# Performance work log

Hardware: AMD Instinct MI355X
Metric: run time of the kernel (lower is better)

## Reference

```python
import jax, jax.numpy as jnp
import numpy as np

N = 500_000
B = 10_000
L = N // B  # 50 tokens per session
H = 128


def setup_inputs() -> dict:
    key = jax.random.key(0)
    ks = jax.random.split(key, 7)
    x = jax.random.normal(ks[0], (N, H), dtype=jnp.float32)
    # sorted segment ids: B sessions of length L (every segment non-empty)
    batch = jnp.repeat(jnp.arange(B, dtype=jnp.int32), L)
    # index of the last element of each session
    last_ixs = jnp.arange(B, dtype=jnp.int32) * L + (L - 1)
    s = 1.0 / np.sqrt(H)
    W1_w = jax.random.uniform(ks[1], (H, H), jnp.float32, -s, s)
    W1_b = jax.random.uniform(ks[2], (H,), jnp.float32, -s, s)
    W2_w = jax.random.uniform(ks[3], (H, H), jnp.float32, -s, s)
    W2_b = jax.random.uniform(ks[4], (H,), jnp.float32, -s, s)
    q_w = jax.random.uniform(ks[5], (1, H), jnp.float32, -s, s)
    q_b = jax.random.uniform(ks[6], (1,), jnp.float32, -s, s)
    return {"x": x, "W1_w": W1_w, "W1_b": W1_b, "W2_w": W2_w, "W2_b": W2_b,
            "q_w": q_w, "q_b": q_b, "batch": batch, "last_ixs": last_ixs,
            "num_segments": B}


def reference(x, W1_w, W1_b, W2_w, W2_b, q_w, q_b, batch, last_ixs, num_segments):
    # v_i = x[last_ixs]; repeat_interleave(v_i, bincount(batch)) == v_i[batch] (batch sorted)
    v_n_repeat = x[last_ixs][batch]                                   # [N, H]
    h = jax.nn.sigmoid(v_n_repeat @ W1_w.T + W1_b + x @ W2_w.T + W2_b)  # [N, H]
    e = (h @ q_w.T + q_b)[:, 0]                                       # [N]
    # segment-wise (per-session) numerically-stable softmax
    m = jax.ops.segment_max(e, batch, num_segments=num_segments)      # [B]
    z = jnp.exp(e - m[batch])                                         # [N]
    denom = jax.ops.segment_sum(z, batch, num_segments=num_segments)  # [B]
    alpha = (z / denom[batch])[:, None]                               # [N, 1]
    # scatter_add pooling of alpha * x over sessions
    s_g = jax.ops.segment_sum(alpha * x, batch, num_segments=num_segments)  # [B, H]
    return s_g
```

## Files before the change

### kernel.cpp

```cpp
#include <hip/hip_runtime.h>

#define H_DIM 128
#define L_SESS 50
#define B_SESS 10000
#define M_PAD 64
#define LDSTR 136
#define PSTR 68

typedef __bf16 bf16x8 __attribute__((ext_vector_type(8)));
typedef float f32x4 __attribute__((ext_vector_type(4)));

static __device__ __forceinline__ unsigned short f2bf(float f) {
  unsigned int u = __float_as_uint(f);
  u += 0x7FFFu + ((u >> 16) & 1u);
  return (unsigned short)(u >> 16);
}
static __device__ __forceinline__ float bf2f(unsigned short h) {
  return __uint_as_float(((unsigned int)h) << 16);
}

__global__ __launch_bounds__(256) void cvt_w2_kernel(
    const float* __restrict__ w2, unsigned short* __restrict__ w2b) {
  int i = blockIdx.x * 256 + threadIdx.x;
  float4 v = ((const float4*)w2)[i];
  ushort4 o;
  o.x = f2bf(v.x); o.y = f2bf(v.y); o.z = f2bf(v.z); o.w = f2bf(v.w);
  *(ushort4*)(w2b + (size_t)i * 4) = o;
}

__global__ __launch_bounds__(256) void sess_u_kernel(
    const float* __restrict__ x, const float* __restrict__ w1,
    const float* __restrict__ w1b, const float* __restrict__ w2bias,
    float* __restrict__ U) {
  __shared__ __attribute__((aligned(16))) unsigned short W1s[H_DIM * LDSTR];
  __shared__ __attribute__((aligned(16))) unsigned short Vs[16 * LDSTR];
  const int t = threadIdx.x;
  const int s0 = blockIdx.x * 16;

  for (int i = t; i < 4096; i += 256) {
    float4 v = ((const float4*)w1)[i];
    int row = i >> 5;
    int col = (i & 31) * 4;
    ushort4 o;
    o.x = f2bf(v.x); o.y = f2bf(v.y); o.z = f2bf(v.z); o.w = f2bf(v.w);
    *(ushort4*)&W1s[row * LDSTR + col] = o;
  }
  for (int i = t; i < 512; i += 256) {
    int j = i >> 5;
    int col = (i & 31) * 4;
    float4 v = ((const float4*)(x + ((size_t)(s0 + j) * L_SESS + (L_SESS - 1)) * H_DIM))[i & 31];
    ushort4 o;
    o.x = f2bf(v.x); o.y = f2bf(v.y); o.z = f2bf(v.z); o.w = f2bf(v.w);
    *(ushort4*)&Vs[j * LDSTR + col] = o;
  }
  __syncthreads();

  const int lane = t & 63, w = t >> 6, q = lane >> 4, c = lane & 15;
  const int n0 = (w * 2) * 16 + c;
  const int n1 = (w * 2 + 1) * 16 + c;
  f32x4 acc0 = {0.f, 0.f, 0.f, 0.f};
  f32x4 acc1 = {0.f, 0.f, 0.f, 0.f};
#pragma unroll
  for (int kt = 0; kt < 4; ++kt) {
    bf16x8 a  = *(const bf16x8*)&Vs[c * LDSTR + kt * 32 + q * 8];
    bf16x8 b0 = *(const bf16x8*)&W1s[n0 * LDSTR + kt * 32 + q * 8];
    bf16x8 b1 = *(const bf16x8*)&W1s[n1 * LDSTR + kt * 32 + q * 8];
    acc0 = __builtin_amdgcn_mfma_f32_16x16x32_bf16(a, b0, acc0, 0, 0, 0);
    acc1 = __builtin_amdgcn_mfma_f32_16x16x32_bf16(a, b1, acc1, 0, 0, 0);
  }
  float bias0 = w1b[n0] + w2bias[n0];
  float bias1 = w1b[n1] + w2bias[n1];
#pragma unroll
  for (int r = 0; r < 4; ++r) {
    int m = q * 4 + r;
    U[(size_t)(s0 + m) * H_DIM + n0] = acc0[r] + bias0;
    U[(size_t)(s0 + m) * H_DIM + n1] = acc1[r] + bias1;
  }
}

__global__ __launch_bounds__(256) void sess_attn_kernel(
    const float* __restrict__ x, const unsigned short* __restrict__ W2b,
    const float* __restrict__ U, const float* __restrict__ qw,
    const float* __restrict__ qb, float* __restrict__ out) {
  __shared__ __attribute__((aligned(16))) unsigned short Wb[H_DIM * LDSTR];
  __shared__ __attribute__((aligned(16))) unsigned short Xb[M_PAD * LDSTR];
  __shared__ float alpha_s[M_PAD];
  float* psc = (float*)Wb;

  const int t = threadIdx.x;
  const int b = blockIdx.x;
  const int lane = t & 63, w = t >> 6, q = lane >> 4, c = lane & 15;
  const int n0 = (w * 2) * 16 + c;
  const int n1 = (w * 2 + 1) * 16 + c;

  const float un0 = U[(size_t)b * H_DIM + n0];
  const float un1 = U[(size_t)b * H_DIM + n1];
  const float qn0 = qw[n0];
  const float qn1 = qw[n1];
  const float qbv = qb[0];

  for (int i = t; i < 2048; i += 256) {
    uint4 v = ((const uint4*)W2b)[i];
    int row = i >> 4;
    int col = (i & 15) * 8;
    *(uint4*)&Wb[row * LDSTR + col] = v;
  }
  const float* xs = x + (size_t)b * (L_SESS * H_DIM);
  for (int i = t; i < 1600; i += 256) {
    float4 v = ((const float4*)xs)[i];
    int row = i >> 5;
    int col = (i & 31) * 4;
    ushort4 o;
    o.x = f2bf(v.x); o.y = f2bf(v.y); o.z = f2bf(v.z); o.w = f2bf(v.w);
    *(ushort4*)&Xb[row * LDSTR + col] = o;
  }
  __syncthreads();

  f32x4 acc[4][2];
  const f32x4 zero4 = {0.f, 0.f, 0.f, 0.f};
#pragma unroll
  for (int mt = 0; mt < 4; ++mt) { acc[mt][0] = zero4; acc[mt][1] = zero4; }
#pragma unroll
  for (int kt = 0; kt < 4; ++kt) {
    bf16x8 a[4];
#pragma unroll
    for (int mt = 0; mt < 4; ++mt)
      a[mt] = *(const bf16x8*)&Xb[(mt * 16 + c) * LDSTR + kt * 32 + q * 8];
    bf16x8 b0 = *(const bf16x8*)&Wb[n0 * LDSTR + kt * 32 + q * 8];
    bf16x8 b1 = *(const bf16x8*)&Wb[n1 * LDSTR + kt * 32 + q * 8];
#pragma unroll
    for (int mt = 0; mt < 4; ++mt) {
      acc[mt][0] = __builtin_amdgcn_mfma_f32_16x16x32_bf16(a[mt], b0, acc[mt][0], 0, 0, 0);
      acc[mt][1] = __builtin_amdgcn_mfma_f32_16x16x32_bf16(a[mt], b1, acc[mt][1], 0, 0, 0);
    }
  }
  __syncthreads();

#pragma unroll
  for (int mt = 0; mt < 4; ++mt) {
#pragma unroll
    for (int r = 0; r < 4; ++r) {
      float t0 = acc[mt][0][r] + un0;
      float t1 = acc[mt][1][r] + un1;
      float h0 = 1.0f / (1.0f + __expf(-t0));
      float h1 = 1.0f / (1.0f + __expf(-t1));
      int row = mt * 16 + q * 4 + r;
      psc[row * PSTR + w * 16 + c] = h0 * qn0 + h1 * qn1;
    }
  }
  __syncthreads();

  if (t < 64) {
    const float4* prow = (const float4*)(psc + t * PSTR);
    float s = 0.f;
#pragma unroll
    for (int j = 0; j < 16; ++j) {
      float4 v4 = prow[j];
      s += (v4.x + v4.y) + (v4.z + v4.w);
    }
    float e = s + qbv;
    float val = (t < L_SESS) ? e : -1.0e30f;
    float mx = val;
#pragma unroll
    for (int off = 32; off > 0; off >>= 1) mx = fmaxf(mx, __shfl_xor(mx, off));
    float z = (t < L_SESS) ? __expf(e - mx) : 0.f;
    float d = z;
#pragma unroll
    for (int off = 32; off > 0; off >>= 1) d += __shfl_xor(d, off);
    alpha_s[t] = z / d;
  }
  __syncthreads();

  if (t < 64) {
    float s0 = 0.f, s1 = 0.f;
    for (int m = 0; m < L_SESS; ++m) {
      unsigned int pv = *(const unsigned int*)&Xb[m * LDSTR + 2 * t];
      float a = alpha_s[m];
      s0 += a * bf2f((unsigned short)(pv & 0xFFFFu));
      s1 += a * bf2f((unsigned short)(pv >> 16));
    }
    float2 o2;
    o2.x = s0;
    o2.y = s1;
    *(float2*)(out + (size_t)b * H_DIM + 2 * t) = o2;
  }
}

extern "C" void kernel_launch(void* const* d_in, const int* in_sizes, int n_in,
                              void* d_out, int out_size, void* d_ws, size_t ws_size,
                              hipStream_t stream) {
  const float* x    = (const float*)d_in[0];
  const float* w1   = (const float*)d_in[1];
  const float* w1b  = (const float*)d_in[2];
  const float* w2   = (const float*)d_in[3];
  const float* w2bi = (const float*)d_in[4];
  const float* qw   = (const float*)d_in[5];
  const float* qb   = (const float*)d_in[6];
  float* out = (float*)d_out;

  unsigned short* W2bf = (unsigned short*)d_ws;
  float* U = out;

  cvt_w2_kernel<<<16, 256, 0, stream>>>(w2, W2bf);
  sess_u_kernel<<<B_SESS / 16, 256, 0, stream>>>(x, w1, w1b, w2bi, U);
  sess_attn_kernel<<<B_SESS, 256, 0, stream>>>(x, W2bf, U, qw, qb, out);
}
```

Before: 423.3 us.

## Fuse session-vector GEMM into attention kernel and keep W2 in registers

Removes the separate sess_u kernel by computing the last-token W1 projection inside each attention block with a small MFMA on the already-staged row 49. W2 fragments now load straight from global memory into registers rather than being staged through a 34KB LDS tile, which cuts LDS use and allows a higher occupancy hint. The partial score reduction moves to warp shuffles, and the final pooling re-reads fp32 x from global memory with all 256 threads. The trade-off is redundant W1 work per session, since only row 0 of each 16-row MFMA tile is used, plus extra global and L2 traffic for the pooling pass and for W1/W2 fragment loads in every block.

```diff
diff --git a/kernel.cpp b/kernel.cpp
--- a/kernel.cpp
+++ b/kernel.cpp
@@ -3,162 +3,111 @@
 #define H_DIM 128
 #define L_SESS 50
 #define B_SESS 10000
-#define M_PAD 64
 #define LDSTR 136
-#define PSTR 68
+#define ESTR 5
 
+typedef __bf16 bf16_t;
 typedef __bf16 bf16x8 __attribute__((ext_vector_type(8)));
 typedef float f32x4 __attribute__((ext_vector_type(4)));
 
-static __device__ __forceinline__ unsigned short f2bf(float f) {
-  unsigned int u = __float_as_uint(f);
-  u += 0x7FFFu + ((u >> 16) & 1u);
-  return (unsigned short)(u >> 16);
-}
-static __device__ __forceinline__ float bf2f(unsigned short h) {
-  return __uint_as_float(((unsigned int)h) << 16);
+__global__ __launch_bounds__(256) void cvt_kernel(
+    const float* __restrict__ w1, const float* __restrict__ w2,
+    const float* __restrict__ w1b, const float* __restrict__ w2bi,
+    unsigned short* __restrict__ wout, float* __restrict__ bias12) {
+  int i = blockIdx.x * 256 + threadIdx.x;
+  float4 v = (i < 4096) ? ((const float4*)w1)[i] : ((const float4*)w2)[i - 4096];
+  union { bf16_t h[4]; ushort4 u4; } tmp;
+  tmp.h[0] = (bf16_t)v.x; tmp.h[1] = (bf16_t)v.y;
+  tmp.h[2] = (bf16_t)v.z; tmp.h[3] = (bf16_t)v.w;
+  *(ushort4*)(wout + (size_t)4 * i) = tmp.u4;
+  if (i < H_DIM) bias12[i] = w1b[i] + w2bi[i];
 }
 
-__global__ __launch_bounds__(256) void cvt_w2_kernel(
-    const float* __restrict__ w2, unsigned short* __restrict__ w2b) {
-  int i = blockIdx.x * 256 + threadIdx.x;
-  float4 v = ((const float4*)w2)[i];
-  ushort4 o;
-  o.x = f2bf(v.x); o.y = f2bf(v.y); o.z = f2bf(v.z); o.w = f2bf(v.w);
-  *(ushort4*)(w2b + (size_t)i * 4) = o;
-}
-
-__global__ __launch_bounds__(256) void sess_u_kernel(
-    const float* __restrict__ x, const float* __restrict__ w1,
-    const float* __restrict__ w1b, const float* __restrict__ w2bias,
-    float* __restrict__ U) {
-  __shared__ __attribute__((aligned(16))) unsigned short W1s[H_DIM * LDSTR];
-  __shared__ __attribute__((aligned(16))) unsigned short Vs[16 * LDSTR];
-  const int t = threadIdx.x;
-  const int s0 = blockIdx.x * 16;
-
-  for (int i = t; i < 4096; i += 256) {
-    float4 v = ((const float4*)w1)[i];
-    int row = i >> 5;
-    int col = (i & 31) * 4;
-    ushort4 o;
-    o.x = f2bf(v.x); o.y = f2bf(v.y); o.z = f2bf(v.z); o.w = f2bf(v.w);
-    *(ushort4*)&W1s[row * LDSTR + col] = o;
-  }
-  for (int i = t; i < 512; i += 256) {
-    int j = i >> 5;
-    int col = (i & 31) * 4;
-    float4 v = ((const float4*)(x + ((size_t)(s0 + j) * L_SESS + (L_SESS - 1)) * H_DIM))[i & 31];
-    ushort4 o;
-    o.x = f2bf(v.x); o.y = f2bf(v.y); o.z = f2bf(v.z); o.w = f2bf(v.w);
-    *(ushort4*)&Vs[j * LDSTR + col] = o;
-  }
-  __syncthreads();
-
-  const int lane = t & 63, w = t >> 6, q = lane >> 4, c = lane & 15;
-  const int n0 = (w * 2) * 16 + c;
-  const int n1 = (w * 2 + 1) * 16 + c;
-  f32x4 acc0 = {0.f, 0.f, 0.f, 0.f};
-  f32x4 acc1 = {0.f, 0.f, 0.f, 0.f};
-#pragma unroll
-  for (int kt = 0; kt < 4; ++kt) {
-    bf16x8 a  = *(const bf16x8*)&Vs[c * LDSTR + kt * 32 + q * 8];
-    bf16x8 b0 = *(const bf16x8*)&W1s[n0 * LDSTR + kt * 32 + q * 8];
-    bf16x8 b1 = *(const bf16x8*)&W1s[n1 * LDSTR + kt * 32 + q * 8];
-    acc0 = __builtin_amdgcn_mfma_f32_16x16x32_bf16(a, b0, acc0, 0, 0, 0);
-    acc1 = __builtin_amdgcn_mfma_f32_16x16x32_bf16(a, b1, acc1, 0, 0, 0);
-  }
-  float bias0 = w1b[n0] + w2bias[n0];
-  float bias1 = w1b[n1] + w2bias[n1];
-#pragma unroll
-  for (int r = 0; r < 4; ++r) {
-    int m = q * 4 + r;
-    U[(size_t)(s0 + m) * H_DIM + n0] = acc0[r] + bias0;
-    U[(size_t)(s0 + m) * H_DIM + n1] = acc1[r] + bias1;
-  }
-}
-
-__global__ __launch_bounds__(256) void sess_attn_kernel(
-    const float* __restrict__ x, const unsigned short* __restrict__ W2b,
-    const float* __restrict__ U, const float* __restrict__ qw,
+__global__ __launch_bounds__(256, 4) void sess_attn_kernel(
+    const float* __restrict__ x, const unsigned short* __restrict__ Wb,
+    const float* __restrict__ bias12, const float* __restrict__ qw,
     const float* __restrict__ qb, float* __restrict__ out) {
-  __shared__ __attribute__((aligned(16))) unsigned short Wb[H_DIM * LDSTR];
-  __shared__ __attribute__((aligned(16))) unsigned short Xb[M_PAD * LDSTR];
-  __shared__ float alpha_s[M_PAD];
-  float* psc = (float*)Wb;
+  __shared__ __attribute__((aligned(16))) unsigned short Xb[64 * LDSTR];
+  __shared__ float epart[64 * ESTR];
+  __shared__ float alpha_s[64];
+  __shared__ float pool_s[H_DIM];
 
   const int t = threadIdx.x;
   const int b = blockIdx.x;
   const int lane = t & 63, w = t >> 6, q = lane >> 4, c = lane & 15;
-  const int n0 = (w * 2) * 16 + c;
-  const int n1 = (w * 2 + 1) * 16 + c;
+  const int n0 = w * 32 + c;
+  const int n1 = w * 32 + 16 + c;
 
-  const float un0 = U[(size_t)b * H_DIM + n0];
-  const float un1 = U[(size_t)b * H_DIM + n1];
-  const float qn0 = qw[n0];
-  const float qn1 = qw[n1];
-  const float qbv = qb[0];
+  const float* xs = x + (size_t)b * (L_SESS * H_DIM);
+  const bf16x8* W1v = (const bf16x8*)(Wb);
+  const bf16x8* W2v = (const bf16x8*)(Wb + 16384);
 
-  for (int i = t; i < 2048; i += 256) {
-    uint4 v = ((const uint4*)W2b)[i];
-    int row = i >> 4;
-    int col = (i & 15) * 8;
-    *(uint4*)&Wb[row * LDSTR + col] = v;
+  bf16x8 bw2[4][2];
+#pragma unroll
+  for (int kt = 0; kt < 4; ++kt) {
+    bw2[kt][0] = W2v[(n0 * H_DIM + kt * 32 + q * 8) >> 3];
+    bw2[kt][1] = W2v[(n1 * H_DIM + kt * 32 + q * 8) >> 3];
   }
-  const float* xs = x + (size_t)b * (L_SESS * H_DIM);
+  const float bias0 = bias12[n0], bias1 = bias12[n1];
+  const float qn0 = qw[n0], qn1 = qw[n1], qbv = qb[0];
+
   for (int i = t; i < 1600; i += 256) {
     float4 v = ((const float4*)xs)[i];
-    int row = i >> 5;
-    int col = (i & 31) * 4;
-    ushort4 o;
-    o.x = f2bf(v.x); o.y = f2bf(v.y); o.z = f2bf(v.z); o.w = f2bf(v.w);
-    *(ushort4*)&Xb[row * LDSTR + col] = o;
+    int row = i >> 5, col = (i & 31) * 4;
+    union { bf16_t h[4]; ushort4 u4; } tmp;
+    tmp.h[0] = (bf16_t)v.x; tmp.h[1] = (bf16_t)v.y;
+    tmp.h[2] = (bf16_t)v.z; tmp.h[3] = (bf16_t)v.w;
+    *(ushort4*)&Xb[row * LDSTR + col] = tmp.u4;
   }
   __syncthreads();
 
+  const f32x4 zero4 = {0.f, 0.f, 0.f, 0.f};
+
+  f32x4 accu[2] = {zero4, zero4};
+#pragma unroll
+  for (int kt = 0; kt < 4; ++kt) {
+    bf16x8 av = *(const bf16x8*)&Xb[49 * LDSTR + kt * 32 + q * 8];
+    accu[0] = __builtin_amdgcn_mfma_f32_16x16x32_bf16(
+        av, W1v[(n0 * H_DIM + kt * 32 + q * 8) >> 3], accu[0], 0, 0, 0);
+    accu[1] = __builtin_amdgcn_mfma_f32_16x16x32_bf16(
+        av, W1v[(n1 * H_DIM + kt * 32 + q * 8) >> 3], accu[1], 0, 0, 0);
+  }
+  const float u0 = accu[0][0] + bias0;
+  const float u1 = accu[1][0] + bias1;
+
   f32x4 acc[4][2];
-  const f32x4 zero4 = {0.f, 0.f, 0.f, 0.f};
 #pragma unroll
   for (int mt = 0; mt < 4; ++mt) { acc[mt][0] = zero4; acc[mt][1] = zero4; }
 #pragma unroll
   for (int kt = 0; kt < 4; ++kt) {
-    bf16x8 a[4];
-#pragma unroll
-    for (int mt = 0; mt < 4; ++mt)
-      a[mt] = *(const bf16x8*)&Xb[(mt * 16 + c) * LDSTR + kt * 32 + q * 8];
-    bf16x8 b0 = *(const bf16x8*)&Wb[n0 * LDSTR + kt * 32 + q * 8];
-    bf16x8 b1 = *(const bf16x8*)&Wb[n1 * LDSTR + kt * 32 + q * 8];
 #pragma unroll
     for (int mt = 0; mt < 4; ++mt) {
-      acc[mt][0] = __builtin_amdgcn_mfma_f32_16x16x32_bf16(a[mt], b0, acc[mt][0], 0, 0, 0);
-      acc[mt][1] = __builtin_amdgcn_mfma_f32_16x16x32_bf16(a[mt], b1, acc[mt][1], 0, 0, 0);
+      bf16x8 a = *(const bf16x8*)&Xb[(mt * 16 + c) * LDSTR + kt * 32 + q * 8];
+      acc[mt][0] = __builtin_amdgcn_mfma_f32_16x16x32_bf16(a, bw2[kt][0], acc[mt][0], 0, 0, 0);
+      acc[mt][1] = __builtin_amdgcn_mfma_f32_16x16x32_bf16(a, bw2[kt][1], acc[mt][1], 0, 0, 0);
     }
   }
-  __syncthreads();
 
 #pragma unroll
   for (int mt = 0; mt < 4; ++mt) {
 #pragma unroll
     for (int r = 0; r < 4; ++r) {
-      float t0 = acc[mt][0][r] + un0;
-      float t1 = acc[mt][1][r] + un1;
+      float t0 = acc[mt][0][r] + u0;
+      float t1 = acc[mt][1][r] + u1;
       float h0 = 1.0f / (1.0f + __expf(-t0));
       float h1 = 1.0f / (1.0f + __expf(-t1));
-      int row = mt * 16 + q * 4 + r;
-      psc[row * PSTR + w * 16 + c] = h0 * qn0 + h1 * qn1;
+      float p = h0 * qn0 + h1 * qn1;
+#pragma unroll
+      for (int off = 1; off <= 8; off <<= 1) p += __shfl_xor(p, off);
+      if (c == 0) epart[(mt * 16 + q * 4 + r) * ESTR + w] = p;
     }
   }
   __syncthreads();
 
   if (t < 64) {
-    const float4* prow = (const float4*)(psc + t * PSTR);
-    float s = 0.f;
+    float e = qbv;
 #pragma unroll
-    for (int j = 0; j < 16; ++j) {
-      float4 v4 = prow[j];
-      s += (v4.x + v4.y) + (v4.z + v4.w);
-    }
-    float e = s + qbv;
+    for (int j = 0; j < 4; ++j) e += epart[t * ESTR + j];
     float val = (t < L_SESS) ? e : -1.0e30f;
     float mx = val;
 #pragma unroll
@@ -171,19 +120,14 @@
   }
   __syncthreads();
 
-  if (t < 64) {
-    float s0 = 0.f, s1 = 0.f;
-    for (int m = 0; m < L_SESS; ++m) {
-      unsigned int pv = *(const unsigned int*)&Xb[m * LDSTR + 2 * t];
-      float a = alpha_s[m];
-      s0 += a * bf2f((unsigned short)(pv & 0xFFFFu));
-      s1 += a * bf2f((unsigned short)(pv >> 16));
-    }
-    float2 o2;
-    o2.x = s0;
-    o2.y = s1;
-    *(float2*)(out + (size_t)b * H_DIM + 2 * t) = o2;
-  }
+  const int col = t & 127, half = t >> 7;
+  const float* xp = xs + (size_t)(half * 25) * H_DIM + col;
+  float s = 0.f;
+#pragma unroll
+  for (int m = 0; m < 25; ++m) s += alpha_s[half * 25 + m] * xp[(size_t)m * H_DIM];
+  if (half) pool_s[col] = s;
+  __syncthreads();
+  if (!half) out[(size_t)b * H_DIM + col] = s + pool_s[col];
 }
 
 extern "C" void kernel_launch(void* const* d_in, const int* in_sizes, int n_in,
@@ -198,10 +142,9 @@
   const float* qb   = (const float*)d_in[6];
   float* out = (float*)d_out;
 
-  unsigned short* W2bf = (unsigned short*)d_ws;
-  float* U = out;
+  unsigned short* Wb = (unsigned short*)d_ws;
+  float* bias12 = (float*)((char*)d_ws + 65536);
 
-  cvt_w2_kernel<<<16, 256, 0, stream>>>(w2, W2bf);
-  sess_u_kernel<<<B_SESS / 16, 256, 0, stream>>>(x, w1, w1b, w2bi, U);
-  sess_attn_kernel<<<B_SESS, 256, 0, stream>>>(x, W2bf, U, qw, qb, out);
+  cvt_kernel<<<32, 256, 0, stream>>>(w1, w2, w1b, w2bi, Wb, bias12);
+  sess_attn_kernel<<<B_SESS, 256, 0, stream>>>(x, Wb, bias12, qw, qb, out);
 }
```

After: 417.5 us. About the same (-1.4%).
